# Performance work log

Hardware: AMD Instinct MI355X
Metric: run time of the kernel (lower is better)

The kernel has to match this reference:

```python
import jax, jax.numpy as jnp
import numpy as np

E = 1024
H = 16
D = E // H  # head_dim = 64


def setup_inputs() -> dict:
    key = jax.random.key(0)
    ks = jax.random.split(key, 8)
    B, S = 4, 1024
    return {
        "query": jax.random.normal(ks[0], (B, S, E), jnp.float32),
        "key": jax.random.normal(ks[1], (B, S, E), jnp.float32),
        "value": jax.random.normal(ks[2], (B, S, E), jnp.float32),
        "attn_gate": jax.random.uniform(ks[3], (B, S, S), jnp.float32),
        "in_proj_weight": jax.random.normal(ks[4], (3 * E, E), jnp.float32) * (1.0 / np.sqrt(2 * E)),
        "in_proj_bias": jax.random.normal(ks[5], (3 * E,), jnp.float32) * 0.02,
        "out_proj_weight": jax.random.normal(ks[6], (E, E), jnp.float32) * (1.0 / np.sqrt(E)),
        "out_proj_bias": jnp.zeros((E,), jnp.float32),
    }


def reference(query, key, value, attn_gate, in_proj_weight, in_proj_bias,
              out_proj_weight, out_proj_bias):
    B, S, _ = query.shape
    wq, wk, wv = jnp.split(in_proj_weight, 3, axis=0)  # each (E, E)
    bq, bk, bv = jnp.split(in_proj_bias, 3, axis=0)

    def proj(x, w, b):
        # x: (B,S,E) -> (B,H,S,D)
        y = jnp.einsum("bse,fe->bsf", x, w) + b
        return y.reshape(B, S, H, D).transpose(0, 2, 1, 3)

    q = proj(query, wq, bq) * (D ** -0.5)
    k = proj(key, wk, bk)
    v = proj(value, wv, bv)

    scores = jnp.einsum("bhqd,bhkd->bhqk", q, k)          # (B,H,S,S)
    w = jax.nn.softmax(scores, axis=-1)
    ctx = jnp.einsum("bhqk,bhkd->bhqd", w, v)              # (B,H,S,D)
    ctx = ctx.transpose(0, 2, 1, 3).reshape(B, S, E)
    attn_output = jnp.einsum("bse,fe->bsf", ctx, out_proj_weight) + out_proj_bias

    # average_attn_weights=True -> mean over heads, then apply gate + renorm
    avg_w = jnp.mean(w, axis=1)                            # (B,S,S)
    gated = avg_w * attn_gate
    gated = gated / (jnp.sum(gated, axis=-1, keepdims=True) + 1e-12)
    return attn_output, gated
```

## Files before the change

### kernel.cpp

```cpp
#include <hip/hip_runtime.h>

typedef unsigned short ushortT;
typedef __attribute__((ext_vector_type(8))) short bf16x8;
typedef __attribute__((ext_vector_type(4))) float f32x4;

constexpr int Ec = 1024;
constexpr int Hc = 16;
constexpr int Dc = 64;
constexpr int Bc = 4;
constexpr int Sc = 1024;
constexpr int XN = Bc * Sc * Ec;
constexpr int LDW = 72;

#define MFMA_BF16 __builtin_amdgcn_mfma_f32_16x16x32_bf16

__device__ __forceinline__ ushortT f2bf(float f) {
  union { float f; unsigned int u; } x{f};
  unsigned int r = x.u + 0x7fffu + ((x.u >> 16) & 1u);
  return (ushortT)(r >> 16);
}

struct US8 { ushortT u[8]; };

__global__ __launch_bounds__(256) void k_cast(
    const float* __restrict__ q, const float* __restrict__ k,
    const float* __restrict__ v, const float* __restrict__ wi,
    const float* __restrict__ wo,
    ushortT* __restrict__ oq, ushortT* __restrict__ ok,
    ushortT* __restrict__ ov, ushortT* __restrict__ owi,
    ushortT* __restrict__ owo)
{
  const int seg = blockIdx.y;
  const float* src; ushortT* dst; int n;
  if      (seg == 0) { src = q;  dst = oq;  n = XN; }
  else if (seg == 1) { src = k;  dst = ok;  n = XN; }
  else if (seg == 2) { src = v;  dst = ov;  n = XN; }
  else if (seg == 3) { src = wi; dst = owi; n = 3 * Ec * Ec; }
  else               { src = wo; dst = owo; n = Ec * Ec; }
  int base = (blockIdx.x * 256 + threadIdx.x) * 8;
  if (base >= n) return;
  float4 a = *reinterpret_cast<const float4*>(src + base);
  float4 b = *reinterpret_cast<const float4*>(src + base + 4);
  US8 o;
  o.u[0] = f2bf(a.x); o.u[1] = f2bf(a.y); o.u[2] = f2bf(a.z); o.u[3] = f2bf(a.w);
  o.u[4] = f2bf(b.x); o.u[5] = f2bf(b.y); o.u[6] = f2bf(b.z); o.u[7] = f2bf(b.w);
  *reinterpret_cast<US8*>(dst + base) = o;
}

__global__ __launch_bounds__(256) void k_qkv_mfma(
    const ushortT* __restrict__ xq, const ushortT* __restrict__ xk,
    const ushortT* __restrict__ xv, const ushortT* __restrict__ wi,
    const float* __restrict__ bias, ushortT* __restrict__ qkv)
{
  __shared__ __align__(16) ushortT As[128][LDW];
  __shared__ __align__(16) ushortT Bs[128][LDW];
  const int tid = threadIdx.x;
  const int lane = tid & 63, wid = tid >> 6;
  const int wm = wid >> 1, wn = wid & 1;
  const int li = lane & 15, gi = lane >> 4;
  const int m0 = blockIdx.x * 128, n0 = blockIdx.y * 128;
  const int third = n0 >> 10;
  const ushortT* x = (third == 0) ? xq : (third == 1) ? xk : xv;

  f32x4 acc[4][4] = {};

  for (int k0 = 0; k0 < 1024; k0 += 64) {
    __syncthreads();
#pragma unroll
    for (int i = 0; i < 4; ++i) {
      int c = tid + i * 256;
      int row = c >> 3, col = (c & 7) * 8;
      *reinterpret_cast<uint4*>(&As[row][col]) =
          *reinterpret_cast<const uint4*>(x + (size_t)(m0 + row) * 1024 + k0 + col);
      *reinterpret_cast<uint4*>(&Bs[row][col]) =
          *reinterpret_cast<const uint4*>(wi + (size_t)(n0 + row) * 1024 + k0 + col);
    }
    __syncthreads();
#pragma unroll
    for (int ks = 0; ks < 2; ++ks) {
      bf16x8 a[4], b[4];
#pragma unroll
      for (int t = 0; t < 4; ++t) {
        a[t] = *reinterpret_cast<const bf16x8*>(&As[wm * 64 + t * 16 + li][ks * 32 + gi * 8]);
        b[t] = *reinterpret_cast<const bf16x8*>(&Bs[wn * 64 + t * 16 + li][ks * 32 + gi * 8]);
      }
#pragma unroll
      for (int mi = 0; mi < 4; ++mi)
#pragma unroll
        for (int ni = 0; ni < 4; ++ni)
          acc[mi][ni] = MFMA_BF16(a[mi], b[ni], acc[mi][ni], 0, 0, 0);
    }
  }

  const float scale = (third == 0) ? 0.125f : 1.0f;
#pragma unroll
  for (int ni = 0; ni < 4; ++ni) {
    int n = n0 + wn * 64 + ni * 16 + li;
    float bv = bias[n];
    int h = (n >> 6) & 15, d = n & 63;
#pragma unroll
    for (int mi = 0; mi < 4; ++mi)
#pragma unroll
      for (int r = 0; r < 4; ++r) {
        int m = m0 + wm * 64 + mi * 16 + gi * 4 + r;
        int b_ = m >> 10, s = m & 1023;
        size_t o = ((((size_t)third * Bc + b_) * Hc + h) * Sc + s) * Dc + d;
        qkv[o] = f2bf((acc[mi][ni][r] + bv) * scale);
      }
  }
}

__global__ __launch_bounds__(256) void k_flash_mfma(
    const ushortT* __restrict__ qkv, ushortT* __restrict__ ctx,
    float* __restrict__ mrow, float* __restrict__ lrow)
{
  __shared__ __align__(16) ushortT Qs[64][LDW];
  __shared__ __align__(16) ushortT Ks[64][LDW];
  __shared__ __align__(16) ushortT Vt[64][LDW];
  __shared__ __align__(16) ushortT Ps[64][LDW];
  const int tid = threadIdx.x;
  const int lane = tid & 63, w = tid >> 6;
  const int li = lane & 15, gi = lane >> 4;
  const int s0 = blockIdx.x * 64;
  const int bh = blockIdx.z * Hc + blockIdx.y;
  const ushortT* Q = qkv;
  const ushortT* K = qkv + (size_t)XN;
  const ushortT* V = qkv + (size_t)2 * XN;
  const size_t bhb = (size_t)bh * Sc * Dc;

#pragma unroll
  for (int i = 0; i < 2; ++i) {
    int c = tid + i * 256;
    int row = c >> 3, col = (c & 7) * 8;
    *reinterpret_cast<uint4*>(&Qs[row][col]) =
        *reinterpret_cast<const uint4*>(Q + bhb + (size_t)(s0 + row) * 64 + col);
  }

  f32x4 oa[4] = {};
  float m_r[4], l_r[4];
#pragma unroll
  for (int r = 0; r < 4; ++r) { m_r[r] = -1e30f; l_r[r] = 0.f; }

  const int vp = tid & 31;
  const int vd0 = (tid >> 5) * 8;
  const int ka = (vp & 15) + (vp >> 4) * 32;
  const int kpb = 8 * (vp & 15) + 4 * (vp >> 4);

  for (int kt = 0; kt < 16; ++kt) {
    const int k0 = kt * 64;
    uint4 kreg[2];
#pragma unroll
    for (int i = 0; i < 2; ++i) {
      int c = tid + i * 256;
      int row = c >> 3, col = (c & 7) * 8;
      kreg[i] = *reinterpret_cast<const uint4*>(K + bhb + (size_t)(k0 + row) * 64 + col);
    }
    uint4 va = *reinterpret_cast<const uint4*>(V + bhb + (size_t)(k0 + ka) * 64 + vd0);
    uint4 vb = *reinterpret_cast<const uint4*>(V + bhb + (size_t)(k0 + ka + 16) * 64 + vd0);
    __syncthreads();
#pragma unroll
    for (int i = 0; i < 2; ++i) {
      int c = tid + i * 256;
      int row = c >> 3, col = (c & 7) * 8;
      *reinterpret_cast<uint4*>(&Ks[row][col]) = kreg[i];
    }
    const ushortT* pa_ = reinterpret_cast<const ushortT*>(&va);
    const ushortT* pb_ = reinterpret_cast<const ushortT*>(&vb);
#pragma unroll
    for (int i = 0; i < 8; ++i) {
      unsigned int u = (unsigned int)pa_[i] | ((unsigned int)pb_[i] << 16);
      *reinterpret_cast<unsigned int*>(
          reinterpret_cast<char*>(&Vt[vd0 + i][0]) + kpb) = u;
    }
    __syncthreads();

    f32x4 sc[4] = {};
#pragma unroll
    for (int ds = 0; ds < 2; ++ds) {
      bf16x8 aq = *reinterpret_cast<const bf16x8*>(&Qs[w * 16 + li][ds * 32 + gi * 8]);
#pragma unroll
      for (int nf = 0; nf < 4; ++nf) {
        bf16x8 bk = *reinterpret_cast<const bf16x8*>(&Ks[nf * 16 + li][ds * 32 + gi * 8]);
        sc[nf] = MFMA_BF16(aq, bk, sc[nf], 0, 0, 0);
      }
    }

    float esc[4];
#pragma unroll
    for (int r = 0; r < 4; ++r) {
      float v = fmaxf(fmaxf(sc[0][r], sc[1][r]), fmaxf(sc[2][r], sc[3][r]));
      v = fmaxf(v, __shfl_xor(v, 1));
      v = fmaxf(v, __shfl_xor(v, 2));
      v = fmaxf(v, __shfl_xor(v, 4));
      v = fmaxf(v, __shfl_xor(v, 8));
      float mnew = fmaxf(m_r[r], v);
      esc[r] = __expf(m_r[r] - mnew);
      m_r[r] = mnew;
    }
    float p[4][4];
#pragma unroll
    for (int r = 0; r < 4; ++r) {
      float s = 0.f;
#pragma unroll
      for (int nf = 0; nf < 4; ++nf) { p[nf][r] = __expf(sc[nf][r] - m_r[r]); s += p[nf][r]; }
      s += __shfl_xor(s, 1); s += __shfl_xor(s, 2);
      s += __shfl_xor(s, 4); s += __shfl_xor(s, 8);
      l_r[r] = l_r[r] * esc[r] + s;
#pragma unroll
      for (int nf = 0; nf < 4; ++nf) oa[nf][r] *= esc[r];
    }
#pragma unroll
    for (int r = 0; r < 4; ++r) {
      unsigned int u0 = (unsigned int)f2bf(p[0][r]) | ((unsigned int)f2bf(p[1][r]) << 16);
      unsigned int u1 = (unsigned int)f2bf(p[2][r]) | ((unsigned int)f2bf(p[3][r]) << 16);
      uint2 uu; uu.x = u0; uu.y = u1;
      *reinterpret_cast<uint2*>(
          reinterpret_cast<char*>(&Ps[w * 16 + gi * 4 + r][0]) + li * 8) = uu;
    }
#pragma unroll
    for (int ks = 0; ks < 2; ++ks) {
      bf16x8 pa = *reinterpret_cast<const bf16x8*>(&Ps[w * 16 + li][ks * 32 + gi * 8]);
#pragma unroll
      for (int nf = 0; nf < 4; ++nf) {
        bf16x8 vv = *reinterpret_cast<const bf16x8*>(&Vt[nf * 16 + li][ks * 32 + gi * 8]);
        oa[nf] = MFMA_BF16(pa, vv, oa[nf], 0, 0, 0);
      }
    }
  }

  float inv[4];
#pragma unroll
  for (int r = 0; r < 4; ++r) inv[r] = 1.0f / l_r[r];
#pragma unroll
  for (int nf = 0; nf < 4; ++nf)
#pragma unroll
    for (int r = 0; r < 4; ++r) {
      int q = s0 + w * 16 + gi * 4 + r;
      ctx[bhb + (size_t)q * 64 + nf * 16 + li] = f2bf(oa[nf][r] * inv[r]);
    }
  if (li == 0) {
#pragma unroll
    for (int r = 0; r < 4; ++r) {
      int q = s0 + w * 16 + gi * 4 + r;
      mrow[(size_t)bh * Sc + q] = m_r[r];
      lrow[(size_t)bh * Sc + q] = l_r[r];
    }
  }
}

__global__ __launch_bounds__(256) void k_outproj_mfma(
    const ushortT* __restrict__ ctx, const ushortT* __restrict__ wo,
    const float* __restrict__ bias, float* __restrict__ out)
{
  __shared__ __align__(16) ushortT As[128][LDW];
  __shared__ __align__(16) ushortT Bs[128][LDW];
  const int tid = threadIdx.x;
  const int lane = tid & 63, wid = tid >> 6;
  const int wm = wid >> 1, wn = wid & 1;
  const int li = lane & 15, gi = lane >> 4;
  const int m0 = blockIdx.x * 128, n0 = blockIdx.y * 128;

  f32x4 acc[4][4] = {};

  for (int k0 = 0; k0 < 1024; k0 += 64) {
    const int h = k0 >> 6;
    __syncthreads();
#pragma unroll
    for (int i = 0; i < 4; ++i) {
      int c = tid + i * 256;
      int row = c >> 3, col = (c & 7) * 8;
      int m = m0 + row;
      int b_ = m >> 10, s = m & 1023;
      *reinterpret_cast<uint4*>(&As[row][col]) =
          *reinterpret_cast<const uint4*>(
              ctx + (((size_t)b_ * Hc + h) * Sc + s) * Dc + col);
      *reinterpret_cast<uint4*>(&Bs[row][col]) =
          *reinterpret_cast<const uint4*>(wo + (size_t)(n0 + row) * 1024 + k0 + col);
    }
    __syncthreads();
#pragma unroll
    for (int ks = 0; ks < 2; ++ks) {
      bf16x8 a[4], b[4];
#pragma unroll
      for (int t = 0; t < 4; ++t) {
        a[t] = *reinterpret_cast<const bf16x8*>(&As[wm * 64 + t * 16 + li][ks * 32 + gi * 8]);
        b[t] = *reinterpret_cast<const bf16x8*>(&Bs[wn * 64 + t * 16 + li][ks * 32 + gi * 8]);
      }
#pragma unroll
      for (int mi = 0; mi < 4; ++mi)
#pragma unroll
        for (int ni = 0; ni < 4; ++ni)
          acc[mi][ni] = MFMA_BF16(a[mi], b[ni], acc[mi][ni], 0, 0, 0);
    }
  }

#pragma unroll
  for (int ni = 0; ni < 4; ++ni) {
    int n = n0 + wn * 64 + ni * 16 + li;
    float bv = bias[n];
#pragma unroll
    for (int mi = 0; mi < 4; ++mi)
#pragma unroll
      for (int r = 0; r < 4; ++r) {
        int m = m0 + wm * 64 + mi * 16 + gi * 4 + r;
        out[(size_t)m * 1024 + n] = acc[mi][ni][r] + bv;
      }
  }
}

__global__ __launch_bounds__(256) void k_avggate_mfma(
    const ushortT* __restrict__ qkv, const float* __restrict__ mrow,
    const float* __restrict__ lrow, const float* __restrict__ gate,
    float* __restrict__ out1)
{
  const int tid = threadIdx.x;
  const int lane = tid & 63, w = tid >> 6;
  const int li = lane & 15, gi = lane >> 4;
  const int c0 = blockIdx.x * 64;
  const int s0 = blockIdx.y * 64;
  const int b = blockIdx.z;
  const ushortT* Q = qkv;
  const ushortT* K = qkv + (size_t)XN;

  const int qrow = s0 + w * 16 + li;
  f32x4 avg[4] = {};

  for (int h = 0; h < Hc; ++h) {
    const size_t bh = (size_t)b * Hc + h;
    const size_t bhb = bh * Sc * Dc;
    float mh[4], liv[4];
#pragma unroll
    for (int r = 0; r < 4; ++r) {
      int q = s0 + w * 16 + gi * 4 + r;
      mh[r] = mrow[bh * Sc + q];
      liv[r] = 0.0625f / lrow[bh * Sc + q];
    }
    const ushortT* Qb = Q + bhb;
    const ushortT* Kb = K + bhb;

    f32x4 sc[4] = {};
#pragma unroll
    for (int ds = 0; ds < 2; ++ds) {
      bf16x8 aq = *reinterpret_cast<const bf16x8*>(
          Qb + (size_t)qrow * 64 + ds * 32 + gi * 8);
#pragma unroll
      for (int nf = 0; nf < 4; ++nf) {
        bf16x8 bk = *reinterpret_cast<const bf16x8*>(
            Kb + (size_t)(c0 + nf * 16 + li) * 64 + ds * 32 + gi * 8);
        sc[nf] = MFMA_BF16(aq, bk, sc[nf], 0, 0, 0);
      }
    }
#pragma unroll
    for (int nf = 0; nf < 4; ++nf)
#pragma unroll
      for (int r = 0; r < 4; ++r)
        avg[nf][r] += __expf(sc[nf][r] - mh[r]) * liv[r];
  }

#pragma unroll
  for (int nf = 0; nf < 4; ++nf)
#pragma unroll
    for (int r = 0; r < 4; ++r) {
      int q = s0 + w * 16 + gi * 4 + r;
      size_t o = ((size_t)b * Sc + q) * Sc + c0 + nf * 16 + li;
      out1[o] = avg[nf][r] * gate[o];
    }
}

__global__ __launch_bounds__(256) void k_renorm(float* __restrict__ out1)
{
  __shared__ float wsum[4];
  const int tid = threadIdx.x;
  float* row = out1 + (size_t)blockIdx.x * Sc;
  float4 v = *reinterpret_cast<const float4*>(row + tid * 4);
  float s = v.x + v.y + v.z + v.w;
#pragma unroll
  for (int off = 1; off < 64; off <<= 1) s += __shfl_xor(s, off);
  if ((tid & 63) == 0) wsum[tid >> 6] = s;
  __syncthreads();
  float inv = 1.0f / (wsum[0] + wsum[1] + wsum[2] + wsum[3] + 1e-12f);
  v.x *= inv; v.y *= inv; v.z *= inv; v.w *= inv;
  *reinterpret_cast<float4*>(row + tid * 4) = v;
}

extern "C" void kernel_launch(void* const* d_in, const int* in_sizes, int n_in,
                              void* d_out, int out_size, void* d_ws, size_t ws_size,
                              hipStream_t stream) {
  const float* query = (const float*)d_in[0];
  const float* key   = (const float*)d_in[1];
  const float* value = (const float*)d_in[2];
  const float* gate  = (const float*)d_in[3];
  const float* w_in  = (const float*)d_in[4];
  const float* b_in  = (const float*)d_in[5];
  const float* w_out = (const float*)d_in[6];
  const float* b_out = (const float*)d_in[7];

  float* out0 = (float*)d_out;
  float* out1 = out0 + (size_t)Bc * Sc * Ec;

  ushortT* xq   = (ushortT*)d_ws;
  ushortT* xk   = xq + (size_t)XN;
  ushortT* xv   = xk + (size_t)XN;
  ushortT* wi   = xv + (size_t)XN;
  ushortT* wo   = wi + (size_t)3 * Ec * Ec;
  ushortT* qkvb = wo + (size_t)Ec * Ec;
  ushortT* ctxb = xq;
  float* mrow = (float*)(qkvb + (size_t)3 * XN);
  float* lrow = mrow + (size_t)Bc * Hc * Sc;

  hipLaunchKernelGGL(k_cast, dim3(2048, 5), dim3(256), 0, stream,
                     query, key, value, w_in, w_out, xq, xk, xv, wi, wo);
  hipLaunchKernelGGL(k_qkv_mfma, dim3(32, 24), dim3(256), 0, stream,
                     xq, xk, xv, wi, b_in, qkvb);
  hipLaunchKernelGGL(k_flash_mfma, dim3(16, 16, 4), dim3(256), 0, stream,
                     qkvb, ctxb, mrow, lrow);
  hipLaunchKernelGGL(k_outproj_mfma, dim3(32, 8), dim3(256), 0, stream,
                     ctxb, wo, b_out, out0);
  hipLaunchKernelGGL(k_avggate_mfma, dim3(16, 16, 4), dim3(256), 0, stream,
                     qkvb, mrow, lrow, gate, out1);
  hipLaunchKernelGGL(k_renorm, dim3(Bc * Sc), dim3(256), 0, stream, out1);
}
```

Measured before the change: 347.1 us.

## Split head-average kernel across head groups with atomic accumulation; fold normalizer into offset

The head-averaged attention-weight kernel now splits the 16 heads into 4 groups across extra blocks, so there are four times as many blocks. Partial sums are combined with float atomicAdd into a pre-zeroed output. The flash kernel stores a single per-row offset (max + log(l) + log(16)), which replaces the divide and multiply with a single subtraction inside exp. Gate multiplication moves into the renorm kernel. This adds a zeroing pass, 4x atomic traffic on the 16MB output, and nondeterministic summation order.

```diff
diff --git a/kernel.cpp b/kernel.cpp
--- a/kernel.cpp
+++ b/kernel.cpp
@@ -47,6 +47,13 @@
   *reinterpret_cast<US8*>(dst + base) = o;
 }
 
+__global__ __launch_bounds__(256) void k_zero(float* __restrict__ out1)
+{
+  int i = (blockIdx.x * 256 + threadIdx.x) * 4;
+  float4 z = {0.f, 0.f, 0.f, 0.f};
+  *reinterpret_cast<float4*>(out1 + i) = z;
+}
+
 __global__ __launch_bounds__(256) void k_qkv_mfma(
     const ushortT* __restrict__ xq, const ushortT* __restrict__ xk,
     const ushortT* __restrict__ xv, const ushortT* __restrict__ wi,
@@ -112,7 +119,7 @@
 
 __global__ __launch_bounds__(256) void k_flash_mfma(
     const ushortT* __restrict__ qkv, ushortT* __restrict__ ctx,
-    float* __restrict__ mrow, float* __restrict__ lrow)
+    float* __restrict__ offrow)
 {
   __shared__ __align__(16) ushortT Qs[64][LDW];
   __shared__ __align__(16) ushortT Ks[64][LDW];
@@ -242,8 +249,7 @@
 #pragma unroll
     for (int r = 0; r < 4; ++r) {
       int q = s0 + w * 16 + gi * 4 + r;
-      mrow[(size_t)bh * Sc + q] = m_r[r];
-      lrow[(size_t)bh * Sc + q] = l_r[r];
+      offrow[(size_t)bh * Sc + q] = m_r[r] + __logf(l_r[r]) + 2.77258872f;
     }
   }
 }
@@ -308,9 +314,8 @@
   }
 }
 
-__global__ __launch_bounds__(256) void k_avggate_mfma(
-    const ushortT* __restrict__ qkv, const float* __restrict__ mrow,
-    const float* __restrict__ lrow, const float* __restrict__ gate,
+__global__ __launch_bounds__(256) void k_avggate_part(
+    const ushortT* __restrict__ qkv, const float* __restrict__ offrow,
     float* __restrict__ out1)
 {
   const int tid = threadIdx.x;
@@ -318,35 +323,34 @@
   const int li = lane & 15, gi = lane >> 4;
   const int c0 = blockIdx.x * 64;
   const int s0 = blockIdx.y * 64;
-  const int b = blockIdx.z;
-  const ushortT* Q = qkv;
-  const ushortT* K = qkv + (size_t)XN;
+  const int b  = blockIdx.z >> 2;
+  const int hg = blockIdx.z & 3;
+  constexpr size_t HS = (size_t)Sc * Dc;
+  const ushortT* Qb = qkv + (size_t)b * Hc * HS;
+  const ushortT* Kb = qkv + (size_t)XN + (size_t)b * Hc * HS;
 
   const int qrow = s0 + w * 16 + li;
+  const int qoff = s0 + w * 16 + gi * 4;
   f32x4 avg[4] = {};
 
-  for (int h = 0; h < Hc; ++h) {
-    const size_t bh = (size_t)b * Hc + h;
-    const size_t bhb = bh * Sc * Dc;
-    float mh[4], liv[4];
-#pragma unroll
-    for (int r = 0; r < 4; ++r) {
-      int q = s0 + w * 16 + gi * 4 + r;
-      mh[r] = mrow[bh * Sc + q];
-      liv[r] = 0.0625f / lrow[bh * Sc + q];
-    }
-    const ushortT* Qb = Q + bhb;
-    const ushortT* Kb = K + bhb;
+  for (int hi = 0; hi < 4; ++hi) {
+    const int h = hg * 4 + hi;
+    const ushortT* Qh = Qb + (size_t)h * HS;
+    const ushortT* Kh = Kb + (size_t)h * HS;
+
+    float4 of = *reinterpret_cast<const float4*>(
+        offrow + ((size_t)b * Hc + h) * Sc + qoff);
+    float ofa[4] = {of.x, of.y, of.z, of.w};
 
     f32x4 sc[4] = {};
 #pragma unroll
     for (int ds = 0; ds < 2; ++ds) {
       bf16x8 aq = *reinterpret_cast<const bf16x8*>(
-          Qb + (size_t)qrow * 64 + ds * 32 + gi * 8);
+          Qh + (size_t)qrow * 64 + ds * 32 + gi * 8);
 #pragma unroll
       for (int nf = 0; nf < 4; ++nf) {
         bf16x8 bk = *reinterpret_cast<const bf16x8*>(
-            Kb + (size_t)(c0 + nf * 16 + li) * 64 + ds * 32 + gi * 8);
+            Kh + (size_t)(c0 + nf * 16 + li) * 64 + ds * 32 + gi * 8);
         sc[nf] = MFMA_BF16(aq, bk, sc[nf], 0, 0, 0);
       }
     }
@@ -354,25 +358,28 @@
     for (int nf = 0; nf < 4; ++nf)
 #pragma unroll
       for (int r = 0; r < 4; ++r)
-        avg[nf][r] += __expf(sc[nf][r] - mh[r]) * liv[r];
+        avg[nf][r] += __expf(sc[nf][r] - ofa[r]);
   }
 
 #pragma unroll
   for (int nf = 0; nf < 4; ++nf)
 #pragma unroll
     for (int r = 0; r < 4; ++r) {
-      int q = s0 + w * 16 + gi * 4 + r;
+      int q = qoff + r;
       size_t o = ((size_t)b * Sc + q) * Sc + c0 + nf * 16 + li;
-      out1[o] = avg[nf][r] * gate[o];
-    }
-}
-
-__global__ __launch_bounds__(256) void k_renorm(float* __restrict__ out1)
+      atomicAdd(&out1[o], avg[nf][r]);
+    }
+}
+
+__global__ __launch_bounds__(256) void k_renorm_gate(
+    float* __restrict__ out1, const float* __restrict__ gate)
 {
   __shared__ float wsum[4];
   const int tid = threadIdx.x;
-  float* row = out1 + (size_t)blockIdx.x * Sc;
-  float4 v = *reinterpret_cast<const float4*>(row + tid * 4);
+  const size_t base = (size_t)blockIdx.x * Sc + tid * 4;
+  float4 v = *reinterpret_cast<const float4*>(out1 + base);
+  float4 g = *reinterpret_cast<const float4*>(gate + base);
+  v.x *= g.x; v.y *= g.y; v.z *= g.z; v.w *= g.w;
   float s = v.x + v.y + v.z + v.w;
 #pragma unroll
   for (int off = 1; off < 64; off <<= 1) s += __shfl_xor(s, off);
@@ -380,7 +387,7 @@
   __syncthreads();
   float inv = 1.0f / (wsum[0] + wsum[1] + wsum[2] + wsum[3] + 1e-12f);
   v.x *= inv; v.y *= inv; v.z *= inv; v.w *= inv;
-  *reinterpret_cast<float4*>(row + tid * 4) = v;
+  *reinterpret_cast<float4*>(out1 + base) = v;
 }
 
 extern "C" void kernel_launch(void* const* d_in, const int* in_sizes, int n_in,
@@ -405,18 +412,19 @@
   ushortT* wo   = wi + (size_t)3 * Ec * Ec;
   ushortT* qkvb = wo + (size_t)Ec * Ec;
   ushortT* ctxb = xq;
-  float* mrow = (float*)(qkvb + (size_t)3 * XN);
-  float* lrow = mrow + (size_t)Bc * Hc * Sc;
-
+  float* offrow = (float*)(qkvb + (size_t)3 * XN);
+
+  hipLaunchKernelGGL(k_zero, dim3(4096), dim3(256), 0, stream, out1);
   hipLaunchKernelGGL(k_cast, dim3(2048, 5), dim3(256), 0, stream,
                      query, key, value, w_in, w_out, xq, xk, xv, wi, wo);
   hipLaunchKernelGGL(k_qkv_mfma, dim3(32, 24), dim3(256), 0, stream,
                      xq, xk, xv, wi, b_in, qkvb);
   hipLaunchKernelGGL(k_flash_mfma, dim3(16, 16, 4), dim3(256), 0, stream,
-                     qkvb, ctxb, mrow, lrow);
+                     qkvb, ctxb, offrow);
   hipLaunchKernelGGL(k_outproj_mfma, dim3(32, 8), dim3(256), 0, stream,
                      ctxb, wo, b_out, out0);
-  hipLaunchKernelGGL(k_avggate_mfma, dim3(16, 16, 4), dim3(256), 0, stream,
-                     qkvb, mrow, lrow, gate, out1);
-  hipLaunchKernelGGL(k_renorm, dim3(Bc * Sc), dim3(256), 0, stream, out1);
-}
+  hipLaunchKernelGGL(k_avggate_part, dim3(16, 16, 16), dim3(256), 0, stream,
+                     qkvb, offrow, out1);
+  hipLaunchKernelGGL(k_renorm_gate, dim3(Bc * Sc), dim3(256), 0, stream,
+                     out1, gate);
+}
```

After: 390.7 us. 12.6% more time.
